# Optimization experiments

Hardware: AMD Instinct MI355X
Metric: run time of the kernel (lower is better)

Reference implementation:

```python
import jax, jax.numpy as jnp
import numpy as np

C_IN = 96          # spectral bands
D2 = 2 * C_IN      # d = 192 (inner dim)
D4 = 4 * D2        # 768 (4-directional scan channels)
N = 16             # SSM state size
DR = 6             # delta_rank = ceil(96/16)
B, H, W = 2, 96, 96  # H,W not in {8,16,32,64} -> s=1 path


def setup_inputs() -> dict:
    key = jax.random.key(0)
    ks = jax.random.split(key, 8)
    g = lambda k, shape, s: jax.random.normal(k, shape, jnp.float32) * s
    return {
        "x": jax.random.normal(ks[0], (B, C_IN, H, W), jnp.float32),
        "W_in": g(ks[1], (C_IN, 2 * D2), 0.05),          # in_proj (in,out)
        "b_in": jnp.zeros((2 * D2,), jnp.float32),
        "w_dw": g(ks[2], (D2, 1, 3, 3), 0.1),            # depthwise conv OIHW
        "b_dw": jnp.zeros((D2,), jnp.float32),
        "A_log": jnp.log(jnp.tile(jnp.arange(1.0, N + 1.0, dtype=jnp.float32), (D4, 1))),
        "Dp": jnp.ones((D4,), jnp.float32),
        "W_x": g(ks[3], (D4, DR + 2 * N), 0.05),         # x_proj, no bias
        "W_delta": g(ks[4], (DR, D4), 0.1),
        "b_delta": g(ks[5], (D4,), 0.1),
        "ln_g": jnp.ones((D2,), jnp.float32),
        "ln_b": jnp.zeros((D2,), jnp.float32),
        "W_out": g(ks[6], (D2, C_IN), 0.05),             # out_proj, no bias
    }


def _selective_scan(u, delta, A, Bm, Cm, Dv):
    # u, delta: [b,L,d4]; Bm, Cm: [b,L,n]; A: [d4,n]; Dv: [d4]
    b, L, d4 = u.shape
    n = A.shape[1]

    def step(h, inps):
        u_t, dt, B_t, C_t = inps                      # [b,d4],[b,d4],[b,n],[b,n]
        dA = jnp.exp(dt[:, :, None] * A)              # [b,d4,n]
        h = dA * h + (dt * u_t)[:, :, None] * B_t[:, None, :]
        y = jnp.einsum('bdn,bn->bd', h, C_t) + Dv * u_t
        return h, y

    h0 = jnp.zeros((b, d4, n), u.dtype)
    xs = (jnp.swapaxes(u, 0, 1), jnp.swapaxes(delta, 0, 1),
          jnp.swapaxes(Bm, 0, 1), jnp.swapaxes(Cm, 0, 1))
    _, ys = jax.lax.scan(step, h0, xs)                # ys: [L,b,d4]
    return jnp.swapaxes(ys, 0, 1)                     # [b,L,d4]


def reference(x, W_in, b_in, w_dw, b_dw, A_log, Dp, W_x, W_delta, b_delta, ln_g, ln_b, W_out):
    b, c, Hh, Ww = x.shape                            # s = 1 (H not in {8,16,32,64})
    d = W_in.shape[1] // 2
    # in_proj on channel-last, chunk into x / gate z
    xz = jnp.einsum('bchw,ce->bhwe', x, W_in) + b_in  # [b,h,w,2d]
    xx, z = jnp.split(xz, 2, axis=-1)
    # depthwise conv + silu
    xc = jnp.transpose(xx, (0, 3, 1, 2))              # [b,d,h,w]
    xc = jax.lax.conv_general_dilated(
        xc, w_dw, (1, 1), 'SAME', feature_group_count=d,
        dimension_numbers=('NCHW', 'OIHW', 'NCHW')) + b_dw[None, :, None, None]
    xc = jax.nn.silu(xc)
    # 4 directional flattenings (with s=1: x1==x2 row-major, x3==x4 reversed)
    L = Hh * Ww
    flat = xc.reshape(b, d, L)
    flipped = xc[:, :, ::-1, ::-1].reshape(b, d, L)
    xl = jnp.swapaxes(jnp.concatenate([flat, flat, flipped, flipped], axis=1), 1, 2)  # [b,L,4d]
    # SSM parameterization
    A = -jnp.exp(A_log)                               # [4d,n]
    x_dbl = xl @ W_x                                  # [b,L,dr+2n]
    dr, n = W_delta.shape[0], A.shape[1]
    dt_r = x_dbl[..., :dr]
    Bm = x_dbl[..., dr:dr + n]
    Cm = x_dbl[..., dr + n:]
    delta = jax.nn.softplus(dt_r @ W_delta + b_delta)  # [b,L,4d]
    y = _selective_scan(xl, delta, A, Bm, Cm, Dp)      # [b,L,4d]
    # merge 4 directions back to spatial
    y = jnp.transpose(y.reshape(b, L, 4, d), (0, 2, 3, 1))  # [b,4,d,L]
    y1 = y[:, 0].reshape(b, d, Hh, Ww)
    y2 = y[:, 1].reshape(b, d, Hh, Ww)
    y3 = y[:, 2].reshape(b, d, Hh, Ww)[:, :, ::-1, ::-1]
    y4 = y[:, 3].reshape(b, d, Hh, Ww)[:, :, ::-1, ::-1]
    yh = jnp.transpose(y1 + y2 + y3 + y4, (0, 2, 3, 1))  # [b,h,w,d]
    # LayerNorm over d
    mu = yh.mean(-1, keepdims=True)
    var = ((yh - mu) ** 2).mean(-1, keepdims=True)
    yn = (yh - mu) * jax.lax.rsqrt(var + 1e-5) * ln_g + ln_b
    out = (yn * jax.nn.silu(z)) @ W_out               # [b,h,w,c]
    return jnp.transpose(out, (0, 3, 1, 2))           # [b,c,h,w]
```

## Files before the change

### kernel.cpp

```cpp
#include <hip/hip_runtime.h>
#include <hip/hip_bf16.h>
#include <math.h>

#define CIN 96
#define D2 192
#define D4 768
#define LL 9216
#define NN 16
#define NCH 288
#define CLEN 32

typedef float v2f __attribute__((ext_vector_type(2)));

#define SZ_Y4SLOT (2u*2u*9216u*192u)
#define SZ_BL    (2u*9216u*192u)
#define SZ_XDBL  (2u*9216u*38u)
#define SZ_S     (2u*4u*288u*192u)
#define SZ_HSLOT (2u*4u*288u*192u*8u)
#define F_Y4     0u
#define F_XX     0u
#define F_ZS     (F_Y4 + SZ_Y4SLOT)
#define F_XT     (F_ZS + SZ_BL)
#define F_XD0    (F_XT + SZ_BL)
#define F_XD1    (F_XD0 + SZ_XDBL)
#define F_XD2    (F_XD1 + SZ_XDBL)
#define F_XD3    (F_XD2 + SZ_XDBL)
#define F_SBUF   (F_XD3 + SZ_XDBL)
#define F_HBUF   (F_SBUF + SZ_S)
#define F_WCOMB  (F_HBUF + SZ_HSLOT)
#define F_A0     (F_WCOMB + 15360u)
#define F_FF     (F_A0 + 768u)

__device__ __forceinline__ float silu_f(float z) {
    return z / (1.0f + __expf(-z));
}

__global__ __launch_bounds__(256) void k1_inproj(
    const float* __restrict__ x, const float* __restrict__ Win,
    const float* __restrict__ bin, const float* __restrict__ Wx,
    const float* __restrict__ Alog, float* __restrict__ wcomb,
    float* __restrict__ A0f, float* __restrict__ Ffl,
    float* __restrict__ xx, __hip_bfloat16* __restrict__ zs)
{
    __shared__ float xs[32][68];
    __shared__ float wsh[32][100];
    int tid = threadIdx.x;
    int bid = blockIdx.x;

    if (bid < 60) {
        int i = bid * 256 + tid;
        if (i < 768) {
            float a0 = -__expf(Alog[i * 16]);
            bool fast = true;
            for (int n = 1; n < 16; n++) {
                float an = -__expf(Alog[i * 16 + n]);
                float tgt = (n + 1) * a0;
                fast = fast && (fabsf(an - tgt) <= 1e-5f * fabsf(tgt));
            }
            A0f[i] = a0;
            Ffl[i] = fast ? 1.f : 0.f;
        }
        int d = i / 80, j = i % 80;
        float v = 0.f;
        if (j < 38) v = Wx[d * 38 + j] + Wx[(d + 192) * 38 + j];
        else if (j >= 40 && j < 78) {
            int jj = j - 40;
            v = Wx[(d + 384) * 38 + jj] + Wx[(d + 576) * 38 + jj];
        }
        wcomb[i] = v;
    }

    int eq = bid & 3;
    int lt = (bid >> 2) % 144;
    int b = bid / 576;
    int l0 = lt * 64;
    int e0 = eq * 96;

    int lg = tid & 15;
    int cg = tid >> 4;
    v2f acc[4][3];
#pragma unroll
    for (int i = 0; i < 4; i++)
#pragma unroll
        for (int p = 0; p < 3; p++) { acc[i][p].x = 0.f; acc[i][p].y = 0.f; }

    for (int kc = 0; kc < 96; kc += 32) {
        __syncthreads();
        for (int i = tid; i < 512; i += 256) {
            int kk = i >> 4, q = i & 15;
            float4 v = *(const float4*)&x[(size_t)(b * 96 + kc + kk) * LL + l0 + q * 4];
            *(float4*)&xs[kk][q * 4] = v;
        }
        for (int i = tid; i < 768; i += 256) {
            int kk = i / 24, q = i - kk * 24;
            float4 v = *(const float4*)&Win[(kc + kk) * 384 + e0 + q * 4];
            *(float4*)&wsh[kk][q * 4] = v;
        }
        __syncthreads();
#pragma unroll 4
        for (int k = 0; k < 32; k++) {
            float4 xv = *(const float4*)&xs[k][lg * 4];
            const v2f* wp = (const v2f*)&wsh[k][cg * 6];
            v2f w0 = wp[0], w1 = wp[1], w2 = wp[2];
            float xa[4] = {xv.x, xv.y, xv.z, xv.w};
#pragma unroll
            for (int i = 0; i < 4; i++) {
                v2f xi; xi.x = xa[i]; xi.y = xa[i];
                acc[i][0] += xi * w0;
                acc[i][1] += xi * w1;
                acc[i][2] += xi * w2;
            }
        }
    }
    if (eq < 2) {
#pragma unroll
        for (int j = 0; j < 6; j++) {
            int e = e0 + cg * 6 + j;
            float bb = bin[e];
            float4 v = {acc[0][j >> 1][j & 1] + bb, acc[1][j >> 1][j & 1] + bb,
                        acc[2][j >> 1][j & 1] + bb, acc[3][j >> 1][j & 1] + bb};
            *(float4*)&xx[(size_t)(b * 192 + e) * LL + l0 + lg * 4] = v;
        }
    } else {
        int zc0 = e0 - 192 + cg * 6;
        float bb[6];
#pragma unroll
        for (int j = 0; j < 6; j++) bb[j] = bin[e0 + cg * 6 + j];
#pragma unroll
        for (int i = 0; i < 4; i++) {
            int l = l0 + lg * 4 + i;
            __hip_bfloat16* zp = &zs[((size_t)b * LL + l) * 192 + zc0];
#pragma unroll
            for (int p = 0; p < 3; p++) {
                __hip_bfloat162 hv = __halves2bfloat162(
                    __float2bfloat16(silu_f(acc[i][p].x + bb[2 * p])),
                    __float2bfloat16(silu_f(acc[i][p].y + bb[2 * p + 1])));
                *(__hip_bfloat162*)&zp[2 * p] = hv;
            }
        }
    }
}

__global__ __launch_bounds__(192) void k2_conv(
    const float* __restrict__ xx, const float* __restrict__ wdw,
    const float* __restrict__ bdw, float* __restrict__ xt)
{
    __shared__ float tile[32][97];
    __shared__ float wsm[32][9];
    __shared__ float bs[32];
    int tid = threadIdx.x;
    int bid = blockIdx.x;
    int h = bid % 96;
    int r = bid / 96;
    int dg = r % 6;
    int b = r / 6;

    for (int i = tid; i < 288; i += 192) wsm[i / 9][i % 9] = wdw[(dg * 32 + i / 9) * 9 + (i % 9)];
    if (tid < 32) bs[tid] = bdw[dg * 32 + tid];
    __syncthreads();

    int w = tid % 96;
    int dhalf = tid / 96;
    for (int p = 0; p < 16; p++) {
        int dsub = 2 * p + dhalf;
        const float* base = xx + (size_t)(b * 192 + dg * 32 + dsub) * LL;
        float acc = bs[dsub];
#pragma unroll
        for (int kh = 0; kh < 3; kh++) {
            int hh = h + kh - 1;
            if (hh < 0 || hh >= 96) continue;
            const float* row = base + hh * 96;
#pragma unroll
            for (int kw = 0; kw < 3; kw++) {
                int ww = w + kw - 1;
                if (ww < 0 || ww >= 96) continue;
                acc += row[ww] * wsm[dsub][kh * 3 + kw];
            }
        }
        tile[dsub][w] = silu_f(acc);
    }
    __syncthreads();
    for (int i = tid; i < 768; i += 192) {
        int q = i & 7, ls = i >> 3;
        float4 v = {tile[q * 4 + 0][ls], tile[q * 4 + 1][ls], tile[q * 4 + 2][ls], tile[q * 4 + 3][ls]};
        *(float4*)&xt[((size_t)b * LL + h * 96 + ls) * 192 + dg * 32 + q * 4] = v;
    }
}

__global__ __launch_bounds__(320) void k3_xdbl(
    const float* __restrict__ xt, const float* __restrict__ wcomb,
    float* __restrict__ xa0, float* __restrict__ xa1,
    float* __restrict__ xb0, float* __restrict__ xb1)
{
    __shared__ float xs[16][68];
    __shared__ float wsh[16][80];
    int tid = threadIdx.x;
    int bid = blockIdx.x;
    int kh = bid & 1;
    int rt = (bid >> 1) % 144;
    int b = bid / 288;
    int r0 = rt * 64;
    int k0 = kh * 96;
    float* __restrict__ xa = kh ? xa1 : xa0;
    float* __restrict__ xb = kh ? xb1 : xb0;

    int rg = tid / 20;
    int cg = tid % 20;
    v2f acc[4][2];
#pragma unroll
    for (int i = 0; i < 4; i++)
#pragma unroll
        for (int p = 0; p < 2; p++) { acc[i][p].x = 0.f; acc[i][p].y = 0.f; }

    for (int kc = 0; kc < 96; kc += 16) {
        __syncthreads();
        if (tid < 256) {
            int row = tid >> 2, dq = tid & 3;
            float4 v = *(const float4*)&xt[((size_t)b * LL + r0 + row) * 192 + k0 + kc + dq * 4];
            xs[dq * 4 + 0][row] = v.x;
            xs[dq * 4 + 1][row] = v.y;
            xs[dq * 4 + 2][row] = v.z;
            xs[dq * 4 + 3][row] = v.w;
        }
        for (int i = tid; i < 16 * 80; i += 320) {
            int d = i / 80, j = i - d * 80;
            wsh[d][j] = wcomb[(k0 + kc + d) * 80 + j];
        }
        __syncthreads();
#pragma unroll
        for (int d = 0; d < 16; d++) {
            float4 xv = *(const float4*)&xs[d][rg * 4];
            float4 wv = *(const float4*)&wsh[d][cg * 4];
            v2f w01; w01.x = wv.x; w01.y = wv.y;
            v2f w23; w23.x = wv.z; w23.y = wv.w;
            float xr[4] = {xv.x, xv.y, xv.z, xv.w};
#pragma unroll
            for (int i = 0; i < 4; i++) {
                v2f xi; xi.x = xr[i]; xi.y = xr[i];
                acc[i][0] += xi * w01;
                acc[i][1] += xi * w23;
            }
        }
    }
    int c0 = cg * 4;
#pragma unroll
    for (int i = 0; i < 4; i++) {
        int la = r0 + rg * 4 + i;
#pragma unroll
        for (int j = 0; j < 4; j++) {
            int col = c0 + j;
            float v = acc[i][j >> 1][j & 1];
            if (col < 38) {
                xa[((size_t)b * LL + la) * 38 + col] = v;
            } else if (col >= 40 && col < 78) {
                int lb = LL - 1 - la;
                xb[((size_t)b * LL + lb) * 38 + (col - 40)] = v;
            }
        }
    }
}

__global__ __launch_bounds__(192, 4) void k4_pass1(
    const float* __restrict__ xt,
    const float* __restrict__ xa0, const float* __restrict__ xa1,
    const float* __restrict__ xb0, const float* __restrict__ xb1,
    const float* __restrict__ Wd, const float* __restrict__ bdl,
    const float* __restrict__ Alog, const float* __restrict__ A0f,
    const float* __restrict__ Ffl,
    float* __restrict__ Sbuf, __hip_bfloat16* __restrict__ Hbuf)
{
    __shared__ float Bt[CLEN][16];
    __shared__ float Dt[CLEN][6];
    int tid = threadIdx.x;
    int bid = blockIdx.x;
    int k = bid % NCH;
    int r = bid / NCH;
    int dir = r & 3;
    int b = r >> 2;
    int l0 = k * CLEN;
    for (int i = tid; i < CLEN * 16; i += 192) {
        int t = i >> 4, n = i & 15;
        size_t rb = ((size_t)b * LL + l0 + t) * 38 + 6 + n;
        Bt[t][n] = (xa0[rb] + xa1[rb]) + (xb0[rb] + xb1[rb]);
    }
    for (int i = tid; i < CLEN * 6; i += 192) {
        int t = i / 6, rr = i - 6 * t;
        size_t rb = ((size_t)b * LL + l0 + t) * 38 + rr;
        Dt[t][rr] = (xa0[rb] + xa1[rb]) + (xb0[rb] + xb1[rb]);
    }
    __syncthreads();
    int c = tid;
    int d4 = dir * 192 + c;
    float a0 = A0f[d4];
    bool fast = (Ffl[d4] != 0.f);
    float wd[6];
#pragma unroll
    for (int rr = 0; rr < 6; rr++) wd[rr] = Wd[rr * 768 + d4];
    float bde = bdl[d4];
    float S = 0.f;
    int start = (dir < 2) ? l0 : (LL - 1 - l0);
    ptrdiff_t stp = (dir < 2) ? 192 : -192;
    const float* up = xt + (size_t)b * LL * 192 + (size_t)start * 192 + c;
    int bd = b * 4 + dir;
    size_t base = (((size_t)bd * NCH + k) * 192 + c) * 16;
    if (fast) {
        v2f h2[8];
#pragma unroll
        for (int n = 0; n < 8; n++) { h2[n].x = 0.f; h2[n].y = 0.f; }
#pragma unroll 2
        for (int t = 0; t < CLEN; t++) {
            float2 d01 = *(const float2*)&Dt[t][0];
            float2 d23 = *(const float2*)&Dt[t][2];
            float2 d45 = *(const float2*)&Dt[t][4];
            float s = bde + d01.x * wd[0] + d01.y * wd[1] + d23.x * wd[2]
                          + d23.y * wd[3] + d45.x * wd[4] + d45.y * wd[5];
            float dt = (s > 20.f) ? s : __logf(1.f + __expf(s));
            S += dt;
            float u = *up; up += stp;
            float du = dt * u;
            float e1 = __expf(dt * a0);
            float e2 = e1 * e1;
            v2f q; q.x = e1; q.y = e2;
            v2f e2v; e2v.x = e2; e2v.y = e2;
            v2f e4v = e2v * e2v;
            v2f q2 = q * e2v;
            v2f du2; du2.x = du; du2.y = du;
#pragma unroll
            for (int g = 0; g < 4; g++) {
                float4 bq = *(const float4*)&Bt[t][4 * g];
                v2f b0; b0.x = bq.x; b0.y = bq.y;
                v2f b1; b1.x = bq.z; b1.y = bq.w;
                h2[2 * g]     = q  * h2[2 * g]     + du2 * b0;
                h2[2 * g + 1] = q2 * h2[2 * g + 1] + du2 * b1;
                if (g < 3) { q *= e4v; q2 *= e4v; }
            }
        }
        __hip_bfloat16* hb = Hbuf + base;
#pragma unroll
        for (int n = 0; n < 8; n++) {
            hb[2 * n]     = __float2bfloat16(h2[n].x);
            hb[2 * n + 1] = __float2bfloat16(h2[n].y);
        }
    } else {
        float h[16];
#pragma unroll
        for (int n = 0; n < 16; n++) h[n] = 0.f;
        for (int t = 0; t < CLEN; t++) {
            float s = bde;
#pragma unroll
            for (int rr = 0; rr < 6; rr++) s += Dt[t][rr] * wd[rr];
            float dt = (s > 20.f) ? s : __logf(1.f + __expf(s));
            S += dt;
            float u = *up; up += stp;
            float du = dt * u;
#pragma unroll
            for (int n = 0; n < 16; n++) {
                float e = __expf(dt * (-__expf(Alog[d4 * 16 + n])));
                h[n] = e * h[n] + du * Bt[t][n];
            }
        }
#pragma unroll
        for (int n = 0; n < 16; n++) Hbuf[base + n] = __float2bfloat16(h[n]);
    }
    Sbuf[((size_t)bd * NCH + k) * 192 + c] = S;
}

__global__ __launch_bounds__(256) void k4_pass2(
    const float* __restrict__ Sbuf, const float* __restrict__ Alog,
    __hip_bfloat16* __restrict__ Hbuf)
{
    int lane = blockIdx.x * 256 + threadIdx.x;
    int bd = lane / 3072;
    int cn = lane % 3072;
    int c = cn >> 4, n = cn & 15;
    int dir = bd & 3;
    float an = -__expf(Alog[(dir * 192 + c) * 16 + n]);
    float h = 0.f;
#pragma unroll 8
    for (int k = 0; k < NCH; k++) {
        size_t sidx = ((size_t)bd * NCH + k) * 192 + c;
        float S = Sbuf[sidx];
        size_t idx = sidx * 16 + n;
        float hl = __bfloat162float(Hbuf[idx]);
        float P = __expf(an * S);
        Hbuf[idx] = __float2bfloat16(h);
        h = P * h + hl;
    }
}

__global__ __launch_bounds__(192, 4) void k4_pass3(
    const float* __restrict__ xt,
    const float* __restrict__ xa0, const float* __restrict__ xa1,
    const float* __restrict__ xb0, const float* __restrict__ xb1,
    const float* __restrict__ Wd, const float* __restrict__ bdl,
    const float* __restrict__ Alog, const float* __restrict__ A0f,
    const float* __restrict__ Ffl, const float* __restrict__ Dp,
    const __hip_bfloat16* __restrict__ Hbuf, __hip_bfloat16* __restrict__ y4)
{
    __shared__ float Bt[CLEN][16];
    __shared__ float Ct[CLEN][16];
    __shared__ float Dt[CLEN][6];
    int tid = threadIdx.x;
    int bid = blockIdx.x;
    int k = bid % NCH;
    int r = bid / NCH;
    int dir = r & 3;
    int b = r >> 2;
    int l0 = k * CLEN;
    for (int i = tid; i < CLEN * 16; i += 192) {
        int t = i >> 4, n = i & 15;
        size_t rb = ((size_t)b * LL + l0 + t) * 38;
        size_t r1 = rb + 6 + n, r2 = rb + 22 + n;
        Bt[t][n] = (xa0[r1] + xa1[r1]) + (xb0[r1] + xb1[r1]);
        Ct[t][n] = (xa0[r2] + xa1[r2]) + (xb0[r2] + xb1[r2]);
    }
    for (int i = tid; i < CLEN * 6; i += 192) {
        int t = i / 6, rr = i - 6 * t;
        size_t rb = ((size_t)b * LL + l0 + t) * 38 + rr;
        Dt[t][rr] = (xa0[rb] + xa1[rb]) + (xb0[rb] + xb1[rb]);
    }
    __syncthreads();
    int c = tid;
    int d4 = dir * 192 + c;
    float a0 = A0f[d4];
    bool fast = (Ffl[d4] != 0.f);
    float wd[6];
#pragma unroll
    for (int rr = 0; rr < 6; rr++) wd[rr] = Wd[rr * 768 + d4];
    float bde = bdl[d4];
    float Dv = Dp[d4];
    int bd = b * 4 + dir;
    size_t base = (((size_t)bd * NCH + k) * 192 + c) * 16;
    int start = (dir < 2) ? l0 : (LL - 1 - l0);
    ptrdiff_t stp = (dir < 2) ? 192 : -192;
    const float* up = xt + (size_t)b * LL * 192 + (size_t)start * 192 + c;
    __hip_bfloat16* yp = y4 + (size_t)bd * LL * 192 + (size_t)start * 192 + c;
    if (fast) {
        v2f h2[8];
        const __hip_bfloat16* hb = Hbuf + base;
#pragma unroll
        for (int n = 0; n < 8; n++) {
            h2[n].x = __bfloat162float(hb[2 * n]);
            h2[n].y = __bfloat162float(hb[2 * n + 1]);
        }
#pragma unroll 2
        for (int t = 0; t < CLEN; t++) {
            float2 d01 = *(const float2*)&Dt[t][0];
            float2 d23 = *(const float2*)&Dt[t][2];
            float2 d45 = *(const float2*)&Dt[t][4];
            float s = bde + d01.x * wd[0] + d01.y * wd[1] + d23.x * wd[2]
                          + d23.y * wd[3] + d45.x * wd[4] + d45.y * wd[5];
            float dt = (s > 20.f) ? s : __logf(1.f + __expf(s));
            float u = *up; up += stp;
            float du = dt * u;
            float e1 = __expf(dt * a0);
            float e2 = e1 * e1;
            v2f q; q.x = e1; q.y = e2;
            v2f e2v; e2v.x = e2; e2v.y = e2;
            v2f e4v = e2v * e2v;
            v2f q2 = q * e2v;
            v2f du2; du2.x = du; du2.y = du;
            v2f ya; ya.x = 0.f; ya.y = 0.f;
            v2f yb; yb.x = 0.f; yb.y = 0.f;
#pragma unroll
            for (int g = 0; g < 4; g++) {
                float4 bq = *(const float4*)&Bt[t][4 * g];
                float4 cq = *(const float4*)&Ct[t][4 * g];
                v2f b0; b0.x = bq.x; b0.y = bq.y;
                v2f b1; b1.x = bq.z; b1.y = bq.w;
                v2f c0v; c0v.x = cq.x; c0v.y = cq.y;
                v2f c1v; c1v.x = cq.z; c1v.y = cq.w;
                h2[2 * g]     = q  * h2[2 * g]     + du2 * b0;
                ya += h2[2 * g] * c0v;
                h2[2 * g + 1] = q2 * h2[2 * g + 1] + du2 * b1;
                yb += h2[2 * g + 1] * c1v;
                if (g < 3) { q *= e4v; q2 *= e4v; }
            }
            float yv = (ya.x + ya.y) + (yb.x + yb.y) + Dv * u;
            *yp = __float2bfloat16(yv); yp += stp;
        }
    } else {
        float h[16];
#pragma unroll
        for (int n = 0; n < 16; n++) h[n] = __bfloat162float(Hbuf[base + n]);
        for (int t = 0; t < CLEN; t++) {
            float s = bde;
#pragma unroll
            for (int rr = 0; rr < 6; rr++) s += Dt[t][rr] * wd[rr];
            float dt = (s > 20.f) ? s : __logf(1.f + __expf(s));
            float u = *up; up += stp;
            float du = dt * u;
            float yv = Dv * u;
#pragma unroll
            for (int n = 0; n < 16; n++) {
                float e = __expf(dt * (-__expf(Alog[d4 * 16 + n])));
                h[n] = e * h[n] + du * Bt[t][n];
                yv += h[n] * Ct[t][n];
            }
            *yp = __float2bfloat16(yv); yp += stp;
        }
    }
}

__global__ __launch_bounds__(256) void k5_out(
    const __hip_bfloat16* __restrict__ y4, const __hip_bfloat16* __restrict__ zs,
    const float* __restrict__ lng, const float* __restrict__ lnb,
    const float* __restrict__ Wout, float* __restrict__ out)
{
    __shared__ float acts[16][196];
    __shared__ float wsh[32][100];
    int tid = threadIdx.x;
    int wv = tid >> 6;
    int lane = tid & 63;
    int gl0 = blockIdx.x * 16;
    int b = gl0 / LL;
    int l0 = gl0 % LL;
    const size_t ds = (size_t)LL * 192;

    for (int i = 0; i < 4; i++) {
        int rrow = wv * 4 + i;
        int l = l0 + rrow;
        float ypr[2][2], zpr[2][2];
        float s1 = 0.f, s2 = 0.f;
#pragma unroll
        for (int kk = 0; kk < 2; kk++) {
            int pair = kk * 64 + lane;
            bool act = (kk == 0) || (lane < 32);
            float y0 = 0.f, y1 = 0.f, z0 = 0.f, z1 = 0.f;
            if (act) {
                int cbase = pair * 2;
                size_t off = ((size_t)(b * 4) * LL + l) * 192 + cbase;
                __hip_bfloat162 v0 = *(const __hip_bfloat162*)&y4[off];
                __hip_bfloat162 v1 = *(const __hip_bfloat162*)&y4[off + ds];
                __hip_bfloat162 v2 = *(const __hip_bfloat162*)&y4[off + 2 * ds];
                __hip_bfloat162 v3 = *(const __hip_bfloat162*)&y4[off + 3 * ds];
                y0 = __bfloat162float(v0.x) + __bfloat162float(v1.x)
                   + __bfloat162float(v2.x) + __bfloat162float(v3.x);
                y1 = __bfloat162float(v0.y) + __bfloat162float(v1.y)
                   + __bfloat162float(v2.y) + __bfloat162float(v3.y);
                __hip_bfloat162 zv = *(const __hip_bfloat162*)&zs[((size_t)b * LL + l) * 192 + cbase];
                z0 = __bfloat162float(zv.x);
                z1 = __bfloat162float(zv.y);
                s1 += y0 + y1;
                s2 += y0 * y0 + y1 * y1;
            }
            ypr[kk][0] = y0; ypr[kk][1] = y1;
            zpr[kk][0] = z0; zpr[kk][1] = z1;
        }
#pragma unroll
        for (int o = 32; o; o >>= 1) {
            s1 += __shfl_xor(s1, o, 64);
            s2 += __shfl_xor(s2, o, 64);
        }
        float mean = s1 * (1.f / 192.f);
        float var = s2 * (1.f / 192.f) - mean * mean;
        float rs = rsqrtf(var + 1e-5f);
#pragma unroll
        for (int kk = 0; kk < 2; kk++) {
            bool act = (kk == 0) || (lane < 32);
            if (act) {
                int cbase = (kk * 64 + lane) * 2;
#pragma unroll
                for (int p = 0; p < 2; p++) {
                    int cc = cbase + p;
                    float yn = (ypr[kk][p] - mean) * rs * lng[cc] + lnb[cc];
                    acts[rrow][cc] = yn * zpr[kk][p];
                }
            }
        }
    }

    int ty = tid & 15;
    int tx = tid >> 4;
    v2f o2[3];
    o2[0].x = 0.f; o2[0].y = 0.f;
    o2[1].x = 0.f; o2[1].y = 0.f;
    o2[2].x = 0.f; o2[2].y = 0.f;

    for (int kc = 0; kc < 192; kc += 32) {
        __syncthreads();
        for (int i = tid; i < 32 * 24; i += 256) {
            int d = i / 24, q = i - d * 24;
            *(float4*)&wsh[d][q * 4] = *(const float4*)&Wout[(kc + d) * 96 + q * 4];
        }
        __syncthreads();
#pragma unroll
        for (int kk = 0; kk < 32; kk++) {
            float av = acts[ty][kc + kk];
            const v2f* wp = (const v2f*)&wsh[kk][tx * 6];
            v2f w0 = wp[0], w1 = wp[1], w2 = wp[2];
            v2f sp; sp.x = av; sp.y = av;
            o2[0] += sp * w0;
            o2[1] += sp * w1;
            o2[2] += sp * w2;
        }
    }
    int l = l0 + ty;
#pragma unroll
    for (int j = 0; j < 6; j++) {
        int n = tx * 6 + j;
        out[((size_t)(b * 96) + n) * LL + l] = o2[j >> 1][j & 1];
    }
}

extern "C" void kernel_launch(void* const* d_in, const int* in_sizes, int n_in,
                              void* d_out, int out_size, void* d_ws, size_t ws_size,
                              hipStream_t stream)
{
    const float* x    = (const float*)d_in[0];
    const float* Win  = (const float*)d_in[1];
    const float* bin  = (const float*)d_in[2];
    const float* wdw  = (const float*)d_in[3];
    const float* bdw  = (const float*)d_in[4];
    const float* Alog = (const float*)d_in[5];
    const float* Dp   = (const float*)d_in[6];
    const float* Wx   = (const float*)d_in[7];
    const float* Wd   = (const float*)d_in[8];
    const float* bdl  = (const float*)d_in[9];
    const float* lng  = (const float*)d_in[10];
    const float* lnb  = (const float*)d_in[11];
    const float* Wout = (const float*)d_in[12];
    float* out = (float*)d_out;

    float* ws    = (float*)d_ws;
    __hip_bfloat16* y4 = (__hip_bfloat16*)(ws + F_Y4);
    float* xx    = ws + F_XX;
    __hip_bfloat16* zs = (__hip_bfloat16*)(ws + F_ZS);
    float* xt    = ws + F_XT;
    float* xd0   = ws + F_XD0;
    float* xd1   = ws + F_XD1;
    float* xd2   = ws + F_XD2;
    float* xd3   = ws + F_XD3;
    float* Sbuf  = ws + F_SBUF;
    __hip_bfloat16* Hbuf = (__hip_bfloat16*)(ws + F_HBUF);
    float* wcomb = ws + F_WCOMB;
    float* A0f   = ws + F_A0;
    float* Ffl   = ws + F_FF;

    k1_inproj<<<1152, 256, 0, stream>>>(x, Win, bin, Wx, Alog, wcomb, A0f, Ffl, xx, zs);
    k2_conv<<<1152, 192, 0, stream>>>(xx, wdw, bdw, xt);
    k3_xdbl<<<576, 320, 0, stream>>>(xt, wcomb, xd0, xd1, xd2, xd3);
    k4_pass1<<<2304, 192, 0, stream>>>(xt, xd0, xd1, xd2, xd3, Wd, bdl, Alog, A0f, Ffl, Sbuf, Hbuf);
    k4_pass2<<<96, 256, 0, stream>>>(Sbuf, Alog, Hbuf);
    k4_pass3<<<2304, 192, 0, stream>>>(xt, xd0, xd1, xd2, xd3, Wd, bdl, Alog, A0f, Ffl, Dp, Hbuf, y4);
    k5_out<<<1152, 256, 0, stream>>>(y4, zs, lng, lnb, Wout, out);
}
```

Before: 284.2 us.

## Process paired scan directions in one thread and sum their outputs

Each thread in the chunked scan passes now handles two directions that share the same input sequence (forward pair or flipped pair). It loads u and the B/C/delta rows once, runs both recurrences, and writes a single summed y, which halves the y workspace. The output kernel then reads two y slots instead of four. The grid is halved and the occupancy hint drops from 4 to 3 because the extra state registers per thread raise register pressure.

```diff
diff --git a/kernel.cpp b/kernel.cpp
--- a/kernel.cpp
+++ b/kernel.cpp
@@ -12,14 +12,14 @@
 
 typedef float v2f __attribute__((ext_vector_type(2)));
 
-#define SZ_Y4SLOT (2u*2u*9216u*192u)
+#define SZ_Y2SLOT (2u*2u*9216u*192u)
 #define SZ_BL    (2u*9216u*192u)
 #define SZ_XDBL  (2u*9216u*38u)
 #define SZ_S     (2u*4u*288u*192u)
 #define SZ_HSLOT (2u*4u*288u*192u*8u)
-#define F_Y4     0u
+#define F_Y2     0u
 #define F_XX     0u
-#define F_ZS     (F_Y4 + SZ_Y4SLOT)
+#define F_ZS     (F_Y2 + SZ_Y2SLOT)
 #define F_XT     (F_ZS + SZ_BL)
 #define F_XD0    (F_XT + SZ_BL)
 #define F_XD1    (F_XD0 + SZ_XDBL)
@@ -260,7 +260,7 @@
     }
 }
 
-__global__ __launch_bounds__(192, 4) void k4_pass1(
+__global__ __launch_bounds__(192, 3) void k4_pass1(
     const float* __restrict__ xt,
     const float* __restrict__ xa0, const float* __restrict__ xa1,
     const float* __restrict__ xb0, const float* __restrict__ xb1,
@@ -275,8 +275,8 @@
     int bid = blockIdx.x;
     int k = bid % NCH;
     int r = bid / NCH;
-    int dir = r & 3;
-    int b = r >> 2;
+    int pair = r & 1;
+    int b = r >> 1;
     int l0 = k * CLEN;
     for (int i = tid; i < CLEN * 16; i += 192) {
         int t = i >> 4, n = i & 15;
@@ -290,79 +290,99 @@
     }
     __syncthreads();
     int c = tid;
-    int d4 = dir * 192 + c;
-    float a0 = A0f[d4];
-    bool fast = (Ffl[d4] != 0.f);
-    float wd[6];
-#pragma unroll
-    for (int rr = 0; rr < 6; rr++) wd[rr] = Wd[rr * 768 + d4];
-    float bde = bdl[d4];
-    float S = 0.f;
-    int start = (dir < 2) ? l0 : (LL - 1 - l0);
-    ptrdiff_t stp = (dir < 2) ? 192 : -192;
+    int dA = (2 * pair) * 192 + c;
+    int dB = dA + 192;
+    float a0A = A0f[dA], a0B = A0f[dB];
+    bool fast = (Ffl[dA] != 0.f) && (Ffl[dB] != 0.f);
+    float wdA[6], wdB[6];
+#pragma unroll
+    for (int rr = 0; rr < 6; rr++) { wdA[rr] = Wd[rr * 768 + dA]; wdB[rr] = Wd[rr * 768 + dB]; }
+    float bdeA = bdl[dA], bdeB = bdl[dB];
+    float SA = 0.f, SB = 0.f;
+    int start = (pair == 0) ? l0 : (LL - 1 - l0);
+    ptrdiff_t stp = (pair == 0) ? 192 : -192;
     const float* up = xt + (size_t)b * LL * 192 + (size_t)start * 192 + c;
-    int bd = b * 4 + dir;
-    size_t base = (((size_t)bd * NCH + k) * 192 + c) * 16;
+    int bdA = b * 4 + 2 * pair, bdB = bdA + 1;
+    size_t baseA = (((size_t)bdA * NCH + k) * 192 + c) * 16;
+    size_t baseB = (((size_t)bdB * NCH + k) * 192 + c) * 16;
     if (fast) {
-        v2f h2[8];
-#pragma unroll
-        for (int n = 0; n < 8; n++) { h2[n].x = 0.f; h2[n].y = 0.f; }
+        v2f hA[8], hB[8];
+#pragma unroll
+        for (int n = 0; n < 8; n++) { hA[n].x = 0.f; hA[n].y = 0.f; hB[n].x = 0.f; hB[n].y = 0.f; }
 #pragma unroll 2
         for (int t = 0; t < CLEN; t++) {
             float2 d01 = *(const float2*)&Dt[t][0];
             float2 d23 = *(const float2*)&Dt[t][2];
             float2 d45 = *(const float2*)&Dt[t][4];
-            float s = bde + d01.x * wd[0] + d01.y * wd[1] + d23.x * wd[2]
-                          + d23.y * wd[3] + d45.x * wd[4] + d45.y * wd[5];
-            float dt = (s > 20.f) ? s : __logf(1.f + __expf(s));
-            S += dt;
+            float sA = bdeA + d01.x * wdA[0] + d01.y * wdA[1] + d23.x * wdA[2]
+                            + d23.y * wdA[3] + d45.x * wdA[4] + d45.y * wdA[5];
+            float sB = bdeB + d01.x * wdB[0] + d01.y * wdB[1] + d23.x * wdB[2]
+                            + d23.y * wdB[3] + d45.x * wdB[4] + d45.y * wdB[5];
+            float dtA = (sA > 20.f) ? sA : __logf(1.f + __expf(sA));
+            float dtB = (sB > 20.f) ? sB : __logf(1.f + __expf(sB));
+            SA += dtA; SB += dtB;
             float u = *up; up += stp;
-            float du = dt * u;
-            float e1 = __expf(dt * a0);
-            float e2 = e1 * e1;
-            v2f q; q.x = e1; q.y = e2;
-            v2f e2v; e2v.x = e2; e2v.y = e2;
-            v2f e4v = e2v * e2v;
-            v2f q2 = q * e2v;
-            v2f du2; du2.x = du; du2.y = du;
+            float duA = dtA * u, duB = dtB * u;
+            float e1A = __expf(dtA * a0A), e1B = __expf(dtB * a0B);
+            float e2A = e1A * e1A, e2B = e1B * e1B;
+            v2f qA; qA.x = e1A; qA.y = e2A;
+            v2f qB; qB.x = e1B; qB.y = e2B;
+            v2f e2vA; e2vA.x = e2A; e2vA.y = e2A;
+            v2f e2vB; e2vB.x = e2B; e2vB.y = e2B;
+            v2f e4vA = e2vA * e2vA, e4vB = e2vB * e2vB;
+            v2f q2A = qA * e2vA, q2B = qB * e2vB;
+            v2f duA2; duA2.x = duA; duA2.y = duA;
+            v2f duB2; duB2.x = duB; duB2.y = duB;
 #pragma unroll
             for (int g = 0; g < 4; g++) {
                 float4 bq = *(const float4*)&Bt[t][4 * g];
                 v2f b0; b0.x = bq.x; b0.y = bq.y;
                 v2f b1; b1.x = bq.z; b1.y = bq.w;
-                h2[2 * g]     = q  * h2[2 * g]     + du2 * b0;
-                h2[2 * g + 1] = q2 * h2[2 * g + 1] + du2 * b1;
-                if (g < 3) { q *= e4v; q2 *= e4v; }
-            }
-        }
-        __hip_bfloat16* hb = Hbuf + base;
+                hA[2 * g]     = qA  * hA[2 * g]     + duA2 * b0;
+                hA[2 * g + 1] = q2A * hA[2 * g + 1] + duA2 * b1;
+                hB[2 * g]     = qB  * hB[2 * g]     + duB2 * b0;
+                hB[2 * g + 1] = q2B * hB[2 * g + 1] + duB2 * b1;
+                if (g < 3) { qA *= e4vA; q2A *= e4vA; qB *= e4vB; q2B *= e4vB; }
+            }
+        }
+        __hip_bfloat16* ha = Hbuf + baseA;
+        __hip_bfloat16* hb = Hbuf + baseB;
 #pragma unroll
         for (int n = 0; n < 8; n++) {
-            hb[2 * n]     = __float2bfloat16(h2[n].x);
-            hb[2 * n + 1] = __float2bfloat16(h2[n].y);
+            ha[2 * n]     = __float2bfloat16(hA[n].x);
+            ha[2 * n + 1] = __float2bfloat16(hA[n].y);
+            hb[2 * n]     = __float2bfloat16(hB[n].x);
+            hb[2 * n + 1] = __float2bfloat16(hB[n].y);
         }
     } else {
-        float h[16];
-#pragma unroll
-        for (int n = 0; n < 16; n++) h[n] = 0.f;
+        float hA[16], hB[16];
+#pragma unroll
+        for (int n = 0; n < 16; n++) { hA[n] = 0.f; hB[n] = 0.f; }
         for (int t = 0; t < CLEN; t++) {
-            float s = bde;
-#pragma unroll
-            for (int rr = 0; rr < 6; rr++) s += Dt[t][rr] * wd[rr];
-            float dt = (s > 20.f) ? s : __logf(1.f + __expf(s));
-            S += dt;
+            float sA = bdeA, sB = bdeB;
+#pragma unroll
+            for (int rr = 0; rr < 6; rr++) { sA += Dt[t][rr] * wdA[rr]; sB += Dt[t][rr] * wdB[rr]; }
+            float dtA = (sA > 20.f) ? sA : __logf(1.f + __expf(sA));
+            float dtB = (sB > 20.f) ? sB : __logf(1.f + __expf(sB));
+            SA += dtA; SB += dtB;
             float u = *up; up += stp;
-            float du = dt * u;
+            float duA = dtA * u, duB = dtB * u;
 #pragma unroll
             for (int n = 0; n < 16; n++) {
-                float e = __expf(dt * (-__expf(Alog[d4 * 16 + n])));
-                h[n] = e * h[n] + du * Bt[t][n];
-            }
-        }
-#pragma unroll
-        for (int n = 0; n < 16; n++) Hbuf[base + n] = __float2bfloat16(h[n]);
-    }
-    Sbuf[((size_t)bd * NCH + k) * 192 + c] = S;
+                float eA = __expf(dtA * (-__expf(Alog[dA * 16 + n])));
+                float eB = __expf(dtB * (-__expf(Alog[dB * 16 + n])));
+                hA[n] = eA * hA[n] + duA * Bt[t][n];
+                hB[n] = eB * hB[n] + duB * Bt[t][n];
+            }
+        }
+#pragma unroll
+        for (int n = 0; n < 16; n++) {
+            Hbuf[baseA + n] = __float2bfloat16(hA[n]);
+            Hbuf[baseB + n] = __float2bfloat16(hB[n]);
+        }
+    }
+    Sbuf[((size_t)bdA * NCH + k) * 192 + c] = SA;
+    Sbuf[((size_t)bdB * NCH + k) * 192 + c] = SB;
 }
 
 __global__ __launch_bounds__(256) void k4_pass2(
@@ -388,14 +408,14 @@
     }
 }
 
-__global__ __launch_bounds__(192, 4) void k4_pass3(
+__global__ __launch_bounds__(192, 3) void k4_pass3(
     const float* __restrict__ xt,
     const float* __restrict__ xa0, const float* __restrict__ xa1,
     const float* __restrict__ xb0, const float* __restrict__ xb1,
     const float* __restrict__ Wd, const float* __restrict__ bdl,
     const float* __restrict__ Alog, const float* __restrict__ A0f,
     const float* __restrict__ Ffl, const float* __restrict__ Dp,
-    const __hip_bfloat16* __restrict__ Hbuf, __hip_bfloat16* __restrict__ y4)
+    const __hip_bfloat16* __restrict__ Hbuf, __hip_bfloat16* __restrict__ y2)
 {
     __shared__ float Bt[CLEN][16];
     __shared__ float Ct[CLEN][16];
@@ -404,8 +424,8 @@
     int bid = blockIdx.x;
     int k = bid % NCH;
     int r = bid / NCH;
-    int dir = r & 3;
-    int b = r >> 2;
+    int pair = r & 1;
+    int b = r >> 1;
     int l0 = k * CLEN;
     for (int i = tid; i < CLEN * 16; i += 192) {
         int t = i >> 4, n = i & 15;
@@ -421,45 +441,56 @@
     }
     __syncthreads();
     int c = tid;
-    int d4 = dir * 192 + c;
-    float a0 = A0f[d4];
-    bool fast = (Ffl[d4] != 0.f);
-    float wd[6];
-#pragma unroll
-    for (int rr = 0; rr < 6; rr++) wd[rr] = Wd[rr * 768 + d4];
-    float bde = bdl[d4];
-    float Dv = Dp[d4];
-    int bd = b * 4 + dir;
-    size_t base = (((size_t)bd * NCH + k) * 192 + c) * 16;
-    int start = (dir < 2) ? l0 : (LL - 1 - l0);
-    ptrdiff_t stp = (dir < 2) ? 192 : -192;
+    int dA = (2 * pair) * 192 + c;
+    int dB = dA + 192;
+    float a0A = A0f[dA], a0B = A0f[dB];
+    bool fast = (Ffl[dA] != 0.f) && (Ffl[dB] != 0.f);
+    float wdA[6], wdB[6];
+#pragma unroll
+    for (int rr = 0; rr < 6; rr++) { wdA[rr] = Wd[rr * 768 + dA]; wdB[rr] = Wd[rr * 768 + dB]; }
+    float bdeA = bdl[dA], bdeB = bdl[dB];
+    float DvS = Dp[dA] + Dp[dB];
+    int bdA = b * 4 + 2 * pair, bdB = bdA + 1;
+    size_t baseA = (((size_t)bdA * NCH + k) * 192 + c) * 16;
+    size_t baseB = (((size_t)bdB * NCH + k) * 192 + c) * 16;
+    int start = (pair == 0) ? l0 : (LL - 1 - l0);
+    ptrdiff_t stp = (pair == 0) ? 192 : -192;
     const float* up = xt + (size_t)b * LL * 192 + (size_t)start * 192 + c;
-    __hip_bfloat16* yp = y4 + (size_t)bd * LL * 192 + (size_t)start * 192 + c;
+    __hip_bfloat16* yp = y2 + ((size_t)(b * 2 + pair)) * LL * 192 + (size_t)start * 192 + c;
     if (fast) {
-        v2f h2[8];
-        const __hip_bfloat16* hb = Hbuf + base;
+        v2f hA[8], hB[8];
+        const __hip_bfloat16* ha = Hbuf + baseA;
+        const __hip_bfloat16* hb = Hbuf + baseB;
 #pragma unroll
         for (int n = 0; n < 8; n++) {
-            h2[n].x = __bfloat162float(hb[2 * n]);
-            h2[n].y = __bfloat162float(hb[2 * n + 1]);
+            hA[n].x = __bfloat162float(ha[2 * n]);
+            hA[n].y = __bfloat162float(ha[2 * n + 1]);
+            hB[n].x = __bfloat162float(hb[2 * n]);
+            hB[n].y = __bfloat162float(hb[2 * n + 1]);
         }
 #pragma unroll 2
         for (int t = 0; t < CLEN; t++) {
             float2 d01 = *(const float2*)&Dt[t][0];
             float2 d23 = *(const float2*)&Dt[t][2];
             float2 d45 = *(const float2*)&Dt[t][4];
-            float s = bde + d01.x * wd[0] + d01.y * wd[1] + d23.x * wd[2]
-                          + d23.y * wd[3] + d45.x * wd[4] + d45.y * wd[5];
-            float dt = (s > 20.f) ? s : __logf(1.f + __expf(s));
+            float sA = bdeA + d01.x * wdA[0] + d01.y * wdA[1] + d23.x * wdA[2]
+                            + d23.y * wdA[3] + d45.x * wdA[4] + d45.y * wdA[5];
+            float sB = bdeB + d01.x * wdB[0] + d01.y * wdB[1] + d23.x * wdB[2]
+                            + d23.y * wdB[3] + d45.x * wdB[4] + d45.y * wdB[5];
+            float dtA = (sA > 20.f) ? sA : __logf(1.f + __expf(sA));
+            float dtB = (sB > 20.f) ? sB : __logf(1.f + __expf(sB));
             float u = *up; up += stp;
-            float du = dt * u;
-            float e1 = __expf(dt * a0);
-            float e2 = e1 * e1;
-            v2f q; q.x = e1; q.y = e2;
-            v2f e2v; e2v.x = e2; e2v.y = e2;
-            v2f e4v = e2v * e2v;
-            v2f q2 = q * e2v;
-            v2f du2; du2.x = du; du2.y = du;
+            float duA = dtA * u, duB = dtB * u;
+            float e1A = __expf(dtA * a0A), e1B = __expf(dtB * a0B);
+            float e2A = e1A * e1A, e2B = e1B * e1B;
+            v2f qA; qA.x = e1A; qA.y = e2A;
+            v2f qB; qB.x = e1B; qB.y = e2B;
+            v2f e2vA; e2vA.x = e2A; e2vA.y = e2A;
+            v2f e2vB; e2vB.x = e2B; e2vB.y = e2B;
+            v2f e4vA = e2vA * e2vA, e4vB = e2vB * e2vB;
+            v2f q2A = qA * e2vA, q2B = qB * e2vB;
+            v2f duA2; duA2.x = duA; duA2.y = duA;
+            v2f duB2; duB2.x = duB; duB2.y = duB;
             v2f ya; ya.x = 0.f; ya.y = 0.f;
             v2f yb; yb.x = 0.f; yb.y = 0.f;
 #pragma unroll
@@ -470,32 +501,40 @@
                 v2f b1; b1.x = bq.z; b1.y = bq.w;
                 v2f c0v; c0v.x = cq.x; c0v.y = cq.y;
                 v2f c1v; c1v.x = cq.z; c1v.y = cq.w;
-                h2[2 * g]     = q  * h2[2 * g]     + du2 * b0;
-                ya += h2[2 * g] * c0v;
-                h2[2 * g + 1] = q2 * h2[2 * g + 1] + du2 * b1;
-                yb += h2[2 * g + 1] * c1v;
-                if (g < 3) { q *= e4v; q2 *= e4v; }
-            }
-            float yv = (ya.x + ya.y) + (yb.x + yb.y) + Dv * u;
+                hA[2 * g]     = qA  * hA[2 * g]     + duA2 * b0;
+                hB[2 * g]     = qB  * hB[2 * g]     + duB2 * b0;
+                ya += (hA[2 * g] + hB[2 * g]) * c0v;
+                hA[2 * g + 1] = q2A * hA[2 * g + 1] + duA2 * b1;
+                hB[2 * g + 1] = q2B * hB[2 * g + 1] + duB2 * b1;
+                yb += (hA[2 * g + 1] + hB[2 * g + 1]) * c1v;
+                if (g < 3) { qA *= e4vA; q2A *= e4vA; qB *= e4vB; q2B *= e4vB; }
+            }
+            float yv = (ya.x + ya.y) + (yb.x + yb.y) + DvS * u;
             *yp = __float2bfloat16(yv); yp += stp;
         }
     } else {
-        float h[16];
-#pragma unroll
-        for (int n = 0; n < 16; n++) h[n] = __bfloat162float(Hbuf[base + n]);
+        float hA[16], hB[16];
+#pragma unroll
+        for (int n = 0; n < 16; n++) {
+            hA[n] = __bfloat162float(Hbuf[baseA + n]);
+            hB[n] = __bfloat162float(Hbuf[baseB + n]);
+        }
         for (int t = 0; t < CLEN; t++) {
-            float s = bde;
-#pragma unroll
-            for (int rr = 0; rr < 6; rr++) s += Dt[t][rr] * wd[rr];
-            float dt = (s > 20.f) ? s : __logf(1.f + __expf(s));
+            float sA = bdeA, sB = bdeB;
+#pragma unroll
+            for (int rr = 0; rr < 6; rr++) { sA += Dt[t][rr] * wdA[rr]; sB += Dt[t][rr] * wdB[rr]; }
+            float dtA = (sA > 20.f) ? sA : __logf(1.f + __expf(sA));
+            float dtB = (sB > 20.f) ? sB : __logf(1.f + __expf(sB));
             float u = *up; up += stp;
-            float du = dt * u;
-            float yv = Dv * u;
+            float duA = dtA * u, duB = dtB * u;
+            float yv = DvS * u;
 #pragma unroll
             for (int n = 0; n < 16; n++) {
-                float e = __expf(dt * (-__expf(Alog[d4 * 16 + n])));
-                h[n] = e * h[n] + du * Bt[t][n];
-                yv += h[n] * Ct[t][n];
+                float eA = __expf(dtA * (-__expf(Alog[dA * 16 + n])));
+                float eB = __expf(dtB * (-__expf(Alog[dB * 16 + n])));
+                hA[n] = eA * hA[n] + duA * Bt[t][n];
+                hB[n] = eB * hB[n] + duB * Bt[t][n];
+                yv += (hA[n] + hB[n]) * Ct[t][n];
             }
             *yp = __float2bfloat16(yv); yp += stp;
         }
@@ -503,7 +542,7 @@
 }
 
 __global__ __launch_bounds__(256) void k5_out(
-    const __hip_bfloat16* __restrict__ y4, const __hip_bfloat16* __restrict__ zs,
+    const __hip_bfloat16* __restrict__ y2, const __hip_bfloat16* __restrict__ zs,
     const float* __restrict__ lng, const float* __restrict__ lnb,
     const float* __restrict__ Wout, float* __restrict__ out)
 {
@@ -529,15 +568,11 @@
             float y0 = 0.f, y1 = 0.f, z0 = 0.f, z1 = 0.f;
             if (act) {
                 int cbase = pair * 2;
-                size_t off = ((size_t)(b * 4) * LL + l) * 192 + cbase;
-                __hip_bfloat162 v0 = *(const __hip_bfloat162*)&y4[off];
-                __hip_bfloat162 v1 = *(const __hip_bfloat162*)&y4[off + ds];
-                __hip_bfloat162 v2 = *(const __hip_bfloat162*)&y4[off + 2 * ds];
-                __hip_bfloat162 v3 = *(const __hip_bfloat162*)&y4[off + 3 * ds];
-                y0 = __bfloat162float(v0.x) + __bfloat162float(v1.x)
-                   + __bfloat162float(v2.x) + __bfloat162float(v3.x);
-                y1 = __bfloat162float(v0.y) + __bfloat162float(v1.y)
-                   + __bfloat162float(v2.y) + __bfloat162float(v3.y);
+                size_t off = ((size_t)(b * 2) * LL + l) * 192 + cbase;
+                __hip_bfloat162 v0 = *(const __hip_bfloat162*)&y2[off];
+                __hip_bfloat162 v1 = *(const __hip_bfloat162*)&y2[off + ds];
+                y0 = __bfloat162float(v0.x) + __bfloat162float(v1.x);
+                y1 = __bfloat162float(v0.y) + __bfloat162float(v1.y);
                 __hip_bfloat162 zv = *(const __hip_bfloat162*)&zs[((size_t)b * LL + l) * 192 + cbase];
                 z0 = __bfloat162float(zv.x);
                 z1 = __bfloat162float(zv.y);
@@ -623,7 +658,7 @@
     float* out = (float*)d_out;
 
     float* ws    = (float*)d_ws;
-    __hip_bfloat16* y4 = (__hip_bfloat16*)(ws + F_Y4);
+    __hip_bfloat16* y2 = (__hip_bfloat16*)(ws + F_Y2);
     float* xx    = ws + F_XX;
     __hip_bfloat16* zs = (__hip_bfloat16*)(ws + F_ZS);
     float* xt    = ws + F_XT;
@@ -640,8 +675,8 @@
     k1_inproj<<<1152, 256, 0, stream>>>(x, Win, bin, Wx, Alog, wcomb, A0f, Ffl, xx, zs);
     k2_conv<<<1152, 192, 0, stream>>>(xx, wdw, bdw, xt);
     k3_xdbl<<<576, 320, 0, stream>>>(xt, wcomb, xd0, xd1, xd2, xd3);
-    k4_pass1<<<2304, 192, 0, stream>>>(xt, xd0, xd1, xd2, xd3, Wd, bdl, Alog, A0f, Ffl, Sbuf, Hbuf);
+    k4_pass1<<<1152, 192, 0, stream>>>(xt, xd0, xd1, xd2, xd3, Wd, bdl, Alog, A0f, Ffl, Sbuf, Hbuf);
     k4_pass2<<<96, 256, 0, stream>>>(Sbuf, Alog, Hbuf);
-    k4_pass3<<<2304, 192, 0, stream>>>(xt, xd0, xd1, xd2, xd3, Wd, bdl, Alog, A0f, Ffl, Dp, Hbuf, y4);
-    k5_out<<<1152, 256, 0, stream>>>(y4, zs, lng, lnb, Wout, out);
-}
+    k4_pass3<<<1152, 192, 0, stream>>>(xt, xd0, xd1, xd2, xd3, Wd, bdl, Alog, A0f, Ffl, Dp, Hbuf, y2);
+    k5_out<<<1152, 256, 0, stream>>>(y2, zs, lng, lnb, Wout, out);
+}
```

Measured after the change: 294.9 us. +3.8%, slower.
